# Kernel tuning notes

Hardware: AMD Instinct MI355X
Metric: run time of the kernel (lower is better)

The kernel has to match this reference:

```python
import jax, jax.numpy as jnp
import numpy as np

NEG_SLOPE = 0.2


def gat_conv(x, src, dst, W, a_src, a_dst, b, concat):
    # x: [N, Fin]; W: [H*C, Fin]; a_src/a_dst: [H, C]; b: [H*C] or [C]
    N = x.shape[0]
    H, C = a_src.shape
    h = (x @ W.T).reshape(N, H, C)                      # per-head transform
    s_n = jnp.sum(h * a_src, axis=-1)                   # [N, H]
    d_n = jnp.sum(h * a_dst, axis=-1)                   # [N, H]
    e = jax.nn.leaky_relu(s_n[src] + d_n[dst], NEG_SLOPE)  # [E, H]
    # segment softmax over incoming edges of each destination node
    m = jax.ops.segment_max(e, dst, num_segments=N)
    m = jnp.where(jnp.isfinite(m), m, 0.0)
    ex = jnp.exp(e - m[dst])
    denom = jax.ops.segment_sum(ex, dst, num_segments=N)
    alpha = ex / (denom[dst] + 1e-16)                    # [E, H]
    msg = h[src] * alpha[:, :, None]                     # [E, H, C]
    out = jax.ops.segment_sum(msg, dst, num_segments=N)  # [N, H, C]
    out = out.reshape(N, H * C) if concat else out.mean(axis=1)
    return out + b


def setup_inputs() -> dict:
    key = jax.random.key(0)
    ks = jax.random.split(key, 16)
    N, E, F, C, H = 50000, 800000, 256, 128, 4
    sc = lambda fan_in: 1.0 / np.sqrt(fan_in)
    inp = {
        "x": jax.random.normal(ks[0], (N, F), dtype=jnp.float32),
        "edge_index": jax.random.randint(ks[1], (2, E), 0, N, dtype=jnp.int64),
        # layer 1: F -> H*C (concat)
        "W1": jax.random.normal(ks[2], (H * C, F), jnp.float32) * sc(F),
        "a_src1": jax.random.normal(ks[3], (H, C), jnp.float32) * sc(C),
        "a_dst1": jax.random.normal(ks[4], (H, C), jnp.float32) * sc(C),
        "b1": jnp.zeros((H * C,), jnp.float32),
        # layer 2: H*C -> H*C (concat)
        "W2": jax.random.normal(ks[5], (H * C, H * C), jnp.float32) * sc(H * C),
        "a_src2": jax.random.normal(ks[6], (H, C), jnp.float32) * sc(C),
        "a_dst2": jax.random.normal(ks[7], (H, C), jnp.float32) * sc(C),
        "b2": jnp.zeros((H * C,), jnp.float32),
        # layer 3: H*C -> C (heads=1, concat=False)
        "W3": jax.random.normal(ks[8], (C, H * C), jnp.float32) * sc(H * C),
        "a_src3": jax.random.normal(ks[9], (1, C), jnp.float32) * sc(C),
        "a_dst3": jax.random.normal(ks[10], (1, C), jnp.float32) * sc(C),
        "b3": jnp.zeros((C,), jnp.float32),
        # allocation head: C -> C//2 -> 1
        "Wh1": jax.random.normal(ks[11], (C // 2, C), jnp.float32) * sc(C),
        "bh1": jnp.zeros((C // 2,), jnp.float32),
        "Wh2": jax.random.normal(ks[12], (1, C // 2), jnp.float32) * sc(C // 2),
        "bh2": jnp.zeros((1,), jnp.float32),
    }
    return inp


def reference(x, edge_index, W1, a_src1, a_dst1, b1, W2, a_src2, a_dst2, b2,
              W3, a_src3, a_dst3, b3, Wh1, bh1, Wh2, bh2):
    N = x.shape[0]
    loops = jnp.arange(N, dtype=edge_index.dtype)
    src = jnp.concatenate([edge_index[0], loops])  # self-loops (PyG default)
    dst = jnp.concatenate([edge_index[1], loops])

    h = gat_conv(x, src, dst, W1, a_src1, a_dst1, b1, concat=True)
    h = jax.nn.elu(h)  # dropout is identity at inference
    h = gat_conv(h, src, dst, W2, a_src2, a_dst2, b2, concat=True)
    h = jax.nn.elu(h)
    embeddings = gat_conv(h, src, dst, W3, a_src3, a_dst3, b3, concat=False)

    z = jax.nn.relu(embeddings @ Wh1.T + bh1)
    allocation_scores = jax.nn.sigmoid(z @ Wh2.T + bh2)
    return embeddings, allocation_scores
```

## Files before the change

kernel.cpp:

```cpp
#include <hip/hip_runtime.h>
#include <math.h>

typedef _Float16 f16;
typedef f16 f16x2 __attribute__((ext_vector_type(2)));
typedef f16 f16x4 __attribute__((ext_vector_type(4)));
typedef f16 f16x8 __attribute__((ext_vector_type(8)));
typedef float f32x4 __attribute__((ext_vector_type(4)));

template <int V> struct VecT;
template <> struct VecT<2> { using T = f16 __attribute__((ext_vector_type(2))); };
template <> struct VecT<4> { using T = f16 __attribute__((ext_vector_type(4))); };
template <> struct VecT<8> { using T = f16 __attribute__((ext_vector_type(8))); };

__device__ __forceinline__ unsigned ordf(float f) {
  unsigned u = __float_as_uint(f);
  return (u >> 31) ? ~u : (u | 0x80000000u);
}
__device__ __forceinline__ float unordf(unsigned u) {
  return (u >> 31) ? __uint_as_float(u & 0x7fffffffu) : __uint_as_float(~u);
}


__global__ void k_count(const int* __restrict__ dstArr, int* __restrict__ cnt,
                        int E, int Et) {
  int i = blockIdx.x * blockDim.x + threadIdx.x;
  if (i >= Et) return;
  int d = (i < E) ? dstArr[i] : (i - E);
  atomicAdd(&cnt[d], 1);
}

__global__ __launch_bounds__(256) void k_scanA(const int* __restrict__ cnt,
                                               int* __restrict__ row_ptr,
                                               int* __restrict__ bsum, int n) {
  __shared__ int part[256];
  int t = threadIdx.x;
  int base = blockIdx.x * 1024 + t * 4;
  int4 v = make_int4(0, 0, 0, 0);
  if (base + 3 < n) v = *(const int4*)&cnt[base];
  else {
    if (base + 0 < n) v.x = cnt[base + 0];
    if (base + 1 < n) v.y = cnt[base + 1];
    if (base + 2 < n) v.z = cnt[base + 2];
    if (base + 3 < n) v.w = cnt[base + 3];
  }
  int s = v.x + v.y + v.z + v.w;
  part[t] = s;
  __syncthreads();
  for (int off = 1; off < 256; off <<= 1) {
    int x = (t >= off) ? part[t - off] : 0;
    __syncthreads();
    part[t] += x;
    __syncthreads();
  }
  int p0 = (t == 0) ? 0 : part[t - 1];
  int p1 = p0 + v.x, p2 = p1 + v.y, p3 = p2 + v.z;
  if (base + 0 < n) row_ptr[base + 0] = p0;
  if (base + 1 < n) row_ptr[base + 1] = p1;
  if (base + 2 < n) row_ptr[base + 2] = p2;
  if (base + 3 < n) row_ptr[base + 3] = p3;
  if (t == 255) bsum[blockIdx.x] = part[255];
}

__global__ __launch_bounds__(1024) void k_scanB(int* __restrict__ bsum, int nb) {
  __shared__ int part[1024];
  int t = threadIdx.x;
  int v = (t < nb) ? bsum[t] : 0;
  part[t] = v;
  __syncthreads();
  for (int off = 1; off < 1024; off <<= 1) {
    int x = (t >= off) ? part[t - off] : 0;
    __syncthreads();
    part[t] += x;
    __syncthreads();
  }
  if (t < nb) bsum[t] = (t == 0) ? 0 : part[t - 1];
  if (t == 1023) bsum[nb] = part[1023];
}

__global__ void k_scanC(int* __restrict__ row_ptr, int* __restrict__ cursor,
                        const int* __restrict__ bsum, int n, int nb) {
  int i = blockIdx.x * blockDim.x + threadIdx.x;
  if (i < n) {
    int v = row_ptr[i] + bsum[i >> 10];
    row_ptr[i] = v;
    cursor[i] = v;
  }
  if (i == n) row_ptr[n] = bsum[nb];
}

__global__ void k_fill(const int* __restrict__ dstArr,
                       const int* __restrict__ srcArr, int* __restrict__ cursor,
                       int* __restrict__ esrc, int E, int Et) {
  int i = blockIdx.x * blockDim.x + threadIdx.x;
  if (i >= Et) return;
  int d, s;
  if (i < E) { d = dstArr[i]; s = srcArr[i]; }
  else       { d = i - E; s = d; }
  int pos = atomicAdd(&cursor[d], 1);
  esrc[pos] = s;
}

__global__ void k_f2h4(const float* s0, f16* d0, int n0,
                       const float* s1, f16* d1, int n1,
                       const float* s2, f16* d2, int n2,
                       const float* s3, f16* d3, int n3) {
  int i = blockIdx.x * blockDim.x + threadIdx.x;
  const float* s; f16* d;
  if (i < n0) { s = s0; d = d0; }
  else if ((i -= n0) < n1) { s = s1; d = d1; }
  else if ((i -= n1) < n2) { s = s2; d = d2; }
  else if ((i -= n2) < n3) { s = s3; d = d3; }
  else return;
  float4 v = ((const float4*)s)[i];
  union { f16 h[4]; double dd; } u;
  u.h[0] = (f16)v.x; u.h[1] = (f16)v.y; u.h[2] = (f16)v.z; u.h[3] = (f16)v.w;
  ((double*)d)[i] = u.dd;
}

__global__ __launch_bounds__(256) void k_hgemm_nt(
    const f16* __restrict__ A, const f16* __restrict__ B,
    f16* __restrict__ C, int M, int Nn, int K, int nbx,
    const float* __restrict__ a_src, const float* __restrict__ a_dst,
    float* __restrict__ sArr, float* __restrict__ dArr,
    unsigned* __restrict__ gmaxU, int H) {
  __shared__ f16 As[3 * 4096];
  __shared__ f16 Bs[3 * 4096];
  int tid = threadIdx.x;
  int wave = tid >> 6, lane = tid & 63;
  int quad = lane >> 4, l16 = lane & 15;

  int nwg = gridDim.x;
  int orig = blockIdx.x;
  int q = nwg >> 3, r = nwg & 7;
  int xcd = orig & 7, pos = orig >> 3;
  int swz = (xcd < r) ? (xcd * (q + 1) + pos)
                      : (r * (q + 1) + (xcd - r) * q + pos);
  int bx = swz % nbx;
  int by = swz / nbx;
  int m0 = by * 128, n0 = bx * 128;
  int wm = (wave & 1) * 64, wn = (wave >> 1) * 64;

  int lr = lane >> 2;
  int lc = lane & 3;
  int chunk = lc ^ ((lr >> 1) & 3);
  int rb0 = wave * 16;
  int rb1 = 64 + wave * 16;
  int ga0 = m0 + rb0 + lr; if (ga0 >= M) ga0 = M - 1;
  int ga1 = m0 + rb1 + lr; if (ga1 >= M) ga1 = M - 1;
  const f16* gA0 = A + (size_t)ga0 * K + chunk * 8;
  const f16* gA1 = A + (size_t)ga1 * K + chunk * 8;
  const f16* gB0 = B + (size_t)(n0 + rb0 + lr) * K + chunk * 8;
  const f16* gB1 = B + (size_t)(n0 + rb1 + lr) * K + chunk * 8;

  int rsw = (quad ^ ((l16 >> 1) & 3)) * 8;
  const f16* Ard[4];
  const f16* Brd[4];
#pragma unroll
  for (int i = 0; i < 4; ++i) {
    Ard[i] = &As[(wm + i * 16 + l16) * 32 + rsw];
    Brd[i] = &Bs[(wn + i * 16 + l16) * 32 + rsw];
  }

  f32x4 acc[4][4];
#pragma unroll
  for (int i = 0; i < 4; ++i)
#pragma unroll
    for (int j = 0; j < 4; ++j) acc[i][j] = (f32x4)(0.f);

#define GLDS(gp, lp)                                                     \
  __builtin_amdgcn_global_load_lds(                                      \
      (const __attribute__((address_space(1))) void*)(gp),               \
      (__attribute__((address_space(3))) void*)(lp), 16, 0, 0)
#define STAGE(buf, kk)                                                   \
  do {                                                                   \
    GLDS(gA0 + (kk), As + (buf) * 4096 + rb0 * 32);                      \
    GLDS(gA1 + (kk), As + (buf) * 4096 + rb1 * 32);                      \
    GLDS(gB0 + (kk), Bs + (buf) * 4096 + rb0 * 32);                      \
    GLDS(gB1 + (kk), Bs + (buf) * 4096 + rb1 * 32);                      \
  } while (0)
#define COMPUTE(bufidx)                                                       \
  do {                                                                        \
    f16x8 af[4], bf[4];                                                       \
    _Pragma("unroll") for (int i_ = 0; i_ < 4; ++i_)                          \
        af[i_] = *(const f16x8*)(Ard[i_] + (bufidx) * 4096);                  \
    _Pragma("unroll") for (int j_ = 0; j_ < 4; ++j_)                          \
        bf[j_] = *(const f16x8*)(Brd[j_] + (bufidx) * 4096);                  \
    _Pragma("unroll") for (int i_ = 0; i_ < 4; ++i_)                          \
        _Pragma("unroll") for (int j_ = 0; j_ < 4; ++j_)                      \
            acc[i_][j_] = __builtin_amdgcn_mfma_f32_16x16x32_f16(             \
                af[i_], bf[j_], acc[i_][j_], 0, 0, 0);                        \
  } while (0)

  int nt = K >> 5;
  STAGE(0, 0);
  STAGE(1, 32);
  int cur = 0, sb = 2;
  for (int t = 0; t + 2 < nt; ++t) {
    STAGE(sb, (t + 2) << 5);
    asm volatile("s_waitcnt vmcnt(8)\n\ts_barrier" ::: "memory");
    COMPUTE(cur);
    asm volatile("s_barrier" ::: "memory");
    cur = (cur == 2) ? 0 : cur + 1;
    sb = (sb == 2) ? 0 : sb + 1;
  }
  asm volatile("s_waitcnt vmcnt(4)\n\ts_barrier" ::: "memory");
  COMPUTE(cur);
  asm volatile("s_barrier" ::: "memory");
  cur = (cur == 2) ? 0 : cur + 1;
  asm volatile("s_waitcnt vmcnt(0)\n\ts_barrier" ::: "memory");
  COMPUTE(cur);
#undef STAGE
#undef GLDS
#undef COMPUTE

#pragma unroll
  for (int i = 0; i < 4; ++i) {
#pragma unroll
    for (int r = 0; r < 4; ++r) {
      int m = m0 + wm + i * 16 + quad * 4 + r;
      if (m < M) {
        f16* Cp = C + (size_t)m * Nn + n0 + wn + l16;
#pragma unroll
        for (int j = 0; j < 4; ++j) Cp[j * 16] = (f16)acc[i][j][r];
      }
    }
  }

  float av[4], ad[4];
#pragma unroll
  for (int j = 0; j < 4; ++j) {
    int col = n0 + wn + l16 + j * 16;
    av[j] = a_src[col];
    ad[j] = a_dst[col];
  }
  float sp[16], dp[16];
#pragma unroll
  for (int i = 0; i < 4; ++i)
#pragma unroll
    for (int r = 0; r < 4; ++r) {
      float ss = 0.f, dd = 0.f;
#pragma unroll
      for (int j = 0; j < 4; ++j) {
        ss += acc[i][j][r] * av[j];
        dd += acc[i][j][r] * ad[j];
      }
#pragma unroll
      for (int msk = 1; msk < 16; msk <<= 1) {
        ss += __shfl_xor(ss, msk);
        dd += __shfl_xor(dd, msk);
      }
      sp[i * 4 + r] = ss;
      dp[i * 4 + r] = dd;
    }

  __syncthreads();
  float* fb = (float*)As;
  int wv = wn >> 6;
  if (l16 == 0) {
#pragma unroll
    for (int i = 0; i < 4; ++i)
#pragma unroll
      for (int r = 0; r < 4; ++r) {
        int row = wm + i * 16 + quad * 4 + r;
        fb[wv * 128 + row] = sp[i * 4 + r];
        fb[256 + wv * 128 + row] = dp[i * 4 + r];
      }
  }
  __syncthreads();
  float sval = -3.0e38f;
  if (tid < 128) {
    int m = m0 + tid;
    if (m < M) {
      float s = fb[tid] + fb[128 + tid];
      float d = fb[256 + tid] + fb[384 + tid];
      int head = n0 >> 7;
      sArr[(size_t)m * H + head] = s;
      dArr[(size_t)m * H + head] = d;
      sval = s;
    }
  }
  float mx = sval;
#pragma unroll
  for (int msk = 32; msk; msk >>= 1) mx = fmaxf(mx, __shfl_xor(mx, msk));
  __syncthreads();
  if (lane == 0) fb[512 + wave] = mx;
  __syncthreads();
  if (tid == 0) {
    float m01 = fmaxf(fb[512], fb[513]);
    atomicMax(&gmaxU[n0 >> 7], ordf(m01));
  }
}

template <int HH, int CT, bool DOELU, typename OutT>
__global__ __launch_bounds__(256) void k_aggregate(
    const f16* __restrict__ hin, const float* __restrict__ sArr,
    const float* __restrict__ dArr, const int* __restrict__ row_ptr,
    const int* __restrict__ esrc, const unsigned* __restrict__ gmaxU,
    const float* __restrict__ bias, OutT* __restrict__ outp, int N, int E) {
  constexpr int VEC = (HH == 1) ? 4 : (CT / 64);
  constexpr int CPER = CT / HH;
  using gvec = typename VecT<VEC>::T;

  __shared__ int2 pairs[4][HH * 66];

  int wave = threadIdx.x >> 6;
  int lane = threadIdx.x & 63;
  int n = blockIdx.x * 4 + wave;
  if (n >= N) return;
  int e0 = row_ptr[n];
  int deg = row_ptr[n + 1] - e0;

  const int myhead = (HH == 1) ? 0 : (lane * VEC) / CPER;
  const int l32 = lane & 31, half = lane >> 5;
  const int laneByte = (HH == 1) ? l32 * 8 : lane * VEC * 2;

  float dloc[HH], mn[HH];
#pragma unroll
  for (int h = 0; h < HH; ++h) {
    dloc[h] = dArr[n * HH + h];
    float m = unordf(gmaxU[h]) + dloc[h];
    mn[h] = (m > 0.f) ? m : 0.2f * m;
  }

  float acc[VEC];
#pragma unroll
  for (int k = 0; k < VEC; ++k) acc[k] = 0.f;
  float dsum[HH];
#pragma unroll
  for (int h = 0; h < HH; ++h) dsum[h] = 0.f;

  int2* pw = &pairs[wave][0];
  const int2* pr = &pairs[wave][myhead * 66];

#define PIDX(g, j) ((HH == 1) ? ((g) * 8 + (j) * 2 + half) : ((g) * 4 + (j)))
#define LOADG(VB, WB, g)                                                      \
  do {                                                                        \
    _Pragma("unroll") for (int j_ = 0; j_ < 4; ++j_) {                        \
      int2 p_ = pr[PIDX(g, j_)];                                              \
      WB[j_] = __int_as_float(p_.y);                                          \
      VB[j_] = *(const gvec*)((const char*)hin + (unsigned)(p_.x + laneByte));\
    }                                                                         \
  } while (0)

#define FMAG(VB, WB)                                                          \
  do {                                                                        \
    _Pragma("unroll") for (int j_ = 0; j_ < 4; ++j_)                          \
        _Pragma("unroll") for (int k_ = 0; k_ < VEC; ++k_)                    \
            acc[k_] += WB[j_] * (float)VB[j_][k_];                            \
  } while (0)

  for (int base = 0; base < deg; base += 64) {
    int cn = min(64, deg - base);

    int soff = 0;
    float w_l[HH];
#pragma unroll
    for (int h = 0; h < HH; ++h) w_l[h] = 0.f;
    if (lane < cn) {
      int s = esrc[e0 + base + lane];
      soff = s * (CT * 2);
      if (HH == 4) {
        float4 sv = ((const float4*)sArr)[s];
        float svv[4] = {sv.x, sv.y, sv.z, sv.w};
#pragma unroll
        for (int h = 0; h < 4; ++h) {
          float e = svv[h] + dloc[h];
          e = (e > 0.f) ? e : 0.2f * e;
          w_l[h] = __expf(e - mn[h]);
        }
      } else {
        float e = sArr[s] + dloc[0];
        e = (e > 0.f) ? e : 0.2f * e;
        w_l[0] = __expf(e - mn[0]);
      }
    }
#pragma unroll
    for (int h = 0; h < HH; ++h) dsum[h] += w_l[h];

#pragma unroll
    for (int h = 0; h < HH; ++h)
      pw[h * 66 + lane] = make_int2(soff, __float_as_int(w_l[h]));
    asm volatile("s_waitcnt lgkmcnt(0)" ::: "memory");

    int cng = (HH == 1) ? ((cn + 7) >> 3) : ((cn + 3) >> 2);
    gvec vA[4], vB[4];
    float wA[4], wB[4];
    LOADG(vA, wA, 0);
    int g = 0;
    while (g + 2 < cng) {
      LOADG(vB, wB, g + 1);
      FMAG(vA, wA);
      LOADG(vA, wA, g + 2);
      FMAG(vB, wB);
      g += 2;
    }
    if (g + 1 < cng) {
      LOADG(vB, wB, g + 1);
      FMAG(vA, wA);
      FMAG(vB, wB);
    } else {
      FMAG(vA, wA);
    }
  }
#undef LOADG
#undef FMAG
#undef PIDX

  if (HH == 1) {
#pragma unroll
    for (int k = 0; k < VEC; ++k) acc[k] += __shfl_xor(acc[k], 32);
  }

  float dn;
  if (HH == 4) {
    float t0 = dsum[0], t1 = dsum[1], t2 = dsum[2], t3 = dsum[3];
#pragma unroll
    for (int m = 1; m < 64; m <<= 1) {
      t0 += __shfl_xor(t0, m);
      t1 += __shfl_xor(t1, m);
      t2 += __shfl_xor(t2, m);
      t3 += __shfl_xor(t3, m);
    }
    dn = (myhead < 2) ? (myhead == 0 ? t0 : t1) : (myhead == 2 ? t2 : t3);
  } else {
    float t0 = dsum[0];
#pragma unroll
    for (int m = 1; m < 64; m <<= 1) t0 += __shfl_xor(t0, m);
    dn = t0;
  }
  dn += 1e-16f;

  if (HH == 1) {
    if (lane < 32) {
      struct alignas(16) OutV { OutT v[4]; } ov;
#pragma unroll
      for (int k = 0; k < 4; ++k) {
        float v = acc[k] / dn + bias[l32 * 4 + k];
        if (DOELU) v = (v > 0.f) ? v : expm1f(v);
        ov.v[k] = (OutT)v;
      }
      *(OutV*)(outp + (size_t)n * CT + l32 * 4) = ov;
    }
  } else {
    struct alignas(sizeof(OutT) * VEC) OutV { OutT v[VEC]; } ov;
#pragma unroll
    for (int k = 0; k < VEC; ++k) {
      float v = acc[k] / dn + bias[lane * VEC + k];
      if (DOELU) v = (v > 0.f) ? v : expm1f(v);
      ov.v[k] = (OutT)v;
    }
    *(OutV*)(outp + (size_t)n * CT + lane * VEC) = ov;
  }
}

__global__ __launch_bounds__(256) void k_head(
    const float* __restrict__ emb, const float* __restrict__ Wh1,
    const float* __restrict__ bh1, const float* __restrict__ Wh2,
    const float* __restrict__ bh2, float* __restrict__ scores, int N) {
  __shared__ float w1s[64 * 132];
  __shared__ float w2s[64];
  __shared__ float b1s[64];
  int t = threadIdx.x;
  for (int i = t; i < 64 * 32; i += 256) {
    int r = i >> 5, c4 = i & 31;
    float4 v = ((const float4*)Wh1)[i];
    *(float4*)&w1s[r * 132 + c4 * 4] = v;
  }
  if (t < 64) { w2s[t] = Wh2[t]; b1s[t] = bh1[t]; }
  __syncthreads();
  float b2v = bh2[0];
  int wave = t >> 6, lane = t & 63;
  int gw = blockIdx.x * 4 + wave;
  int nw = gridDim.x * 4;
  for (int n = gw; n < N; n += nw) {
    float2 xv = ((const float2*)(emb + (size_t)n * 128))[lane];
    float z = b1s[lane];
#pragma unroll
    for (int j = 0; j < 32; ++j) {
      float4 w = *(const float4*)&w1s[lane * 132 + 4 * j];
      float a0 = __shfl(xv.x, 2 * j);
      float a1 = __shfl(xv.y, 2 * j);
      float a2 = __shfl(xv.x, 2 * j + 1);
      float a3 = __shfl(xv.y, 2 * j + 1);
      z += w.x * a0 + w.y * a1 + w.z * a2 + w.w * a3;
    }
    z = fmaxf(z, 0.f);
    float v = z * w2s[lane];
#pragma unroll
    for (int off = 32; off; off >>= 1) v += __shfl_down(v, off);
    if (lane == 0) scores[n] = 1.f / (1.f + __expf(-(v + b2v)));
  }
}


extern "C" void kernel_launch(void* const* d_in, const int* in_sizes, int n_in,
                              void* d_out, int out_size, void* d_ws, size_t ws_size,
                              hipStream_t stream) {
  const float* x   = (const float*)d_in[0];
  const int*   ei  = (const int*)d_in[1];
  const float* W1  = (const float*)d_in[2];
  const float* as1 = (const float*)d_in[3];
  const float* ad1 = (const float*)d_in[4];
  const float* b1  = (const float*)d_in[5];
  const float* W2  = (const float*)d_in[6];
  const float* as2 = (const float*)d_in[7];
  const float* ad2 = (const float*)d_in[8];
  const float* b2  = (const float*)d_in[9];
  const float* W3  = (const float*)d_in[10];
  const float* as3 = (const float*)d_in[11];
  const float* ad3 = (const float*)d_in[12];
  const float* b3  = (const float*)d_in[13];
  const float* Wh1 = (const float*)d_in[14];
  const float* bh1 = (const float*)d_in[15];
  const float* Wh2 = (const float*)d_in[16];
  const float* bh2 = (const float*)d_in[17];
  float* out = (float*)d_out;

  const int F = 256, HC = 512, H = 4, C = 128;
  const int N = in_sizes[0] / F;
  const int E = in_sizes[1] / 2;
  const int Et = E + N;
  const int* srcArr = ei;
  const int* dstArr = ei + E;

  char* ws = (char*)d_ws;
  size_t off = 0;
  auto alloc = [&](size_t bytes) -> void* {
    void* p = ws + off;
    off += (bytes + 255) & ~(size_t)255;
    return p;
  };
  f16*   h16    = (f16*)alloc((size_t)N * HC * 2);
  f16*   hAgg   = (f16*)alloc((size_t)N * HC * 2);
  f16*   xh     = (f16*)alloc((size_t)N * F * 2);
  f16*   W1h    = (f16*)alloc((size_t)HC * F * 2);
  f16*   W2h    = (f16*)alloc((size_t)HC * HC * 2);
  f16*   W3h    = (f16*)alloc((size_t)C * HC * 2);
  int* row_ptr  = (int*)alloc((size_t)(N + 1) * 4);
  char* zr      = (char*)alloc((size_t)N * 4 + 64);
  int* cnt      = (int*)zr;
  unsigned* gm1 = (unsigned*)(zr + (size_t)N * 4);
  unsigned* gm2 = gm1 + 4;
  unsigned* gm3 = gm1 + 8;
  int* cursor   = (int*)alloc((size_t)N * 4);
  int* esrc     = (int*)alloc((size_t)Et * 4);
  float* sArr   = (float*)alloc((size_t)N * H * 4);
  float* dArr   = (float*)alloc((size_t)N * H * 4);
  int* bsum     = (int*)alloc((size_t)1028 * 4);
  (void)ws_size; (void)n_in; (void)out_size;

  hipMemsetAsync(zr, 0, (size_t)N * 4 + 64, stream);
  int eb = (Et + 255) / 256;
  int nb = (N + 1023) / 1024;
  k_count<<<eb, 256, 0, stream>>>(dstArr, cnt, E, Et);
  k_scanA<<<nb, 256, 0, stream>>>(cnt, row_ptr, bsum, N);
  k_scanB<<<1, 1024, 0, stream>>>(bsum, nb);
  k_scanC<<<(N + 256) / 256, 256, 0, stream>>>(row_ptr, cursor, bsum, N, nb);
  k_fill<<<eb, 256, 0, stream>>>(dstArr, srcArr, cursor, esrc, E, Et);

  int c0 = N * F / 4, c1 = HC * F / 4, c2 = HC * HC / 4, c3 = C * HC / 4;
  int ctot = c0 + c1 + c2 + c3;
  k_f2h4<<<(ctot + 255) / 256, 256, 0, stream>>>(x, xh, c0, W1, W1h, c1,
                                                 W2, W2h, c2, W3, W3h, c3);

  int aggGrid = (N + 3) / 4;
  int mblk = (N + 127) / 128;
  int nblk1 = 4 * mblk;
  int nblk3 = mblk;

  k_hgemm_nt<<<nblk1, 256, 0, stream>>>(xh, W1h, h16, N, HC, F, 4,
                                        as1, ad1, sArr, dArr, gm1, H);
  k_aggregate<4, 512, true, f16><<<aggGrid, 256, 0, stream>>>(
      h16, sArr, dArr, row_ptr, esrc, gm1, b1, hAgg, N, E);

  k_hgemm_nt<<<nblk1, 256, 0, stream>>>(hAgg, W2h, h16, N, HC, HC, 4,
                                        as2, ad2, sArr, dArr, gm2, H);
  k_aggregate<4, 512, true, f16><<<aggGrid, 256, 0, stream>>>(
      h16, sArr, dArr, row_ptr, esrc, gm2, b2, hAgg, N, E);

  k_hgemm_nt<<<nblk3, 256, 0, stream>>>(hAgg, W3h, h16, N, C, HC, 1,
                                        as3, ad3, sArr, dArr, gm3, 1);
  k_aggregate<1, 128, false, float><<<aggGrid, 256, 0, stream>>>(
      h16, sArr, dArr, row_ptr, esrc, gm3, b3, out, N, E);

  k_head<<<512, 256, 0, stream>>>(out, Wh1, bh1, Wh2, bh2, out + (size_t)N * C, N);
}
```

Measured before the change: 743.5 us.

## Reorder layer-1 GAT to aggregate raw features before the linear transform

For layer 1, the attention logits are computed directly from x by folding a_src/a_dst into W1 (k_ws, k_sd). The raw 256-wide features are then aggregated per head into a [N,4,256] buffer (k_aggx). The per-head GEMM then runs on the aggregated features, with bias and ELU fused into its epilogue. Gathering 256-wide fp16 rows instead of 512-wide transformed rows cuts gather traffic, but it writes and reads a 1024-wide intermediate and adds several kernels.

```diff
diff --git a/kernel.cpp b/kernel.cpp
--- a/kernel.cpp
+++ b/kernel.cpp
@@ -117,10 +117,197 @@
   ((double*)d)[i] = u.dd;
 }
 
+__global__ __launch_bounds__(256) void k_ws(const float* __restrict__ W1,
+                                            const float* __restrict__ as,
+                                            const float* __restrict__ ad,
+                                            float* __restrict__ wsb) {
+  int b = blockIdx.x;
+  int which = b >> 2, h = b & 3;
+  int f = threadIdx.x;
+  const float* av = (which ? ad : as) + h * 128;
+  float acc = 0.f;
+  for (int c = 0; c < 128; ++c)
+    acc += av[c] * W1[(size_t)(h * 128 + c) * 256 + f];
+  wsb[(which * 4 + h) * 256 + f] = acc;
+}
+
+__global__ __launch_bounds__(256) void k_sd(
+    const f16* __restrict__ xh, const float* __restrict__ wsb,
+    float* __restrict__ sArr, float* __restrict__ dArr,
+    unsigned* __restrict__ gmaxU, int N) {
+  __shared__ float mred[4][8];
+  int tid = threadIdx.x;
+  int wave = tid >> 6, lane = tid & 63;
+  float wreg[8][4];
+#pragma unroll
+  for (int q = 0; q < 8; ++q) {
+    float4 w = *(const float4*)&wsb[q * 256 + lane * 4];
+    wreg[q][0] = w.x; wreg[q][1] = w.y; wreg[q][2] = w.z; wreg[q][3] = w.w;
+  }
+  int qsel = lane & 7;
+  float rmax = -3.0e38f;
+  int step = gridDim.x * 4;
+  for (int n = blockIdx.x * 4 + wave; n < N; n += step) {
+    f16x4 xr = *(const f16x4*)(xh + (size_t)n * 256 + lane * 4);
+    float xv[4];
+#pragma unroll
+    for (int k = 0; k < 4; ++k) xv[k] = (float)xr[k];
+    float p[8];
+#pragma unroll
+    for (int q = 0; q < 8; ++q)
+      p[q] = xv[0] * wreg[q][0] + xv[1] * wreg[q][1] +
+             xv[2] * wreg[q][2] + xv[3] * wreg[q][3];
+#pragma unroll
+    for (int m = 1; m < 8; m <<= 1)
+#pragma unroll
+      for (int q = 0; q < 8; ++q) p[q] += __shfl_xor(p[q], m);
+    float s01 = (qsel & 1) ? p[1] : p[0], s23 = (qsel & 1) ? p[3] : p[2];
+    float s45 = (qsel & 1) ? p[5] : p[4], s67 = (qsel & 1) ? p[7] : p[6];
+    float t0 = (qsel & 2) ? s23 : s01, t1 = (qsel & 2) ? s67 : s45;
+    float v = (qsel & 4) ? t1 : t0;
+    v += __shfl_xor(v, 8);
+    v += __shfl_xor(v, 16);
+    v += __shfl_xor(v, 32);
+    if (lane < 4) {
+      sArr[(size_t)n * 4 + lane] = v;
+      rmax = fmaxf(rmax, v);
+    } else if (lane < 8) {
+      dArr[(size_t)n * 4 + (lane - 4)] = v;
+    }
+  }
+  if (lane < 4) mred[wave][lane] = rmax;
+  __syncthreads();
+  if (tid < 4) {
+    float m = fmaxf(fmaxf(mred[0][tid], mred[1][tid]),
+                    fmaxf(mred[2][tid], mred[3][tid]));
+    atomicMax(&gmaxU[tid], ordf(m));
+  }
+}
+
+__global__ __launch_bounds__(256) void k_aggx(
+    const f16* __restrict__ xh, const float* __restrict__ sArr,
+    const float* __restrict__ dArr, const int* __restrict__ row_ptr,
+    const int* __restrict__ esrc, const unsigned* __restrict__ gmaxU,
+    f16* __restrict__ outp, int N, int E) {
+  __shared__ int soffA[4][72];
+  __shared__ float4 w4A[4][64];
+  int wave = threadIdx.x >> 6;
+  int lane = threadIdx.x & 63;
+  int n = blockIdx.x * 4 + wave;
+  if (n >= N) return;
+  int e0 = row_ptr[n];
+  int deg = row_ptr[n + 1] - e0;
+
+  float4 dl4 = ((const float4*)dArr)[n];
+  float dloc[4] = {dl4.x, dl4.y, dl4.z, dl4.w};
+  float mn[4];
+#pragma unroll
+  for (int h = 0; h < 4; ++h) {
+    float m = unordf(gmaxU[h]) + dloc[h];
+    mn[h] = (m > 0.f) ? m : 0.2f * m;
+  }
+
+  float acc[4][4];
+#pragma unroll
+  for (int h = 0; h < 4; ++h)
+#pragma unroll
+    for (int k = 0; k < 4; ++k) acc[h][k] = 0.f;
+  float dsum[4] = {0.f, 0.f, 0.f, 0.f};
+
+  int* so = soffA[wave];
+  float4* wp = w4A[wave];
+
+#define LOADX(VB, WB, g)                                                    \
+  do {                                                                      \
+    _Pragma("unroll") for (int j_ = 0; j_ < 4; ++j_) {                      \
+      int sidx_ = (g) * 4 + j_;                                             \
+      WB[j_] = wp[sidx_];                                                   \
+      VB[j_] = *(const f16x4*)((const char*)xh +                            \
+                               (unsigned)(so[sidx_] + lane * 8));           \
+    }                                                                       \
+  } while (0)
+
+#define FMAX4(VB, WB)                                                       \
+  do {                                                                      \
+    _Pragma("unroll") for (int j_ = 0; j_ < 4; ++j_)                        \
+        _Pragma("unroll") for (int k_ = 0; k_ < 4; ++k_) {                  \
+          float xv_ = (float)VB[j_][k_];                                    \
+          acc[0][k_] += WB[j_].x * xv_;                                     \
+          acc[1][k_] += WB[j_].y * xv_;                                     \
+          acc[2][k_] += WB[j_].z * xv_;                                     \
+          acc[3][k_] += WB[j_].w * xv_;                                     \
+        }                                                                   \
+  } while (0)
+
+  for (int base = 0; base < deg; base += 64) {
+    int cn = min(64, deg - base);
+    int soff = 0;
+    float w_l[4] = {0.f, 0.f, 0.f, 0.f};
+    if (lane < cn) {
+      int s = esrc[e0 + base + lane];
+      soff = s * 512;
+      float4 sv = ((const float4*)sArr)[s];
+      float svv[4] = {sv.x, sv.y, sv.z, sv.w};
+#pragma unroll
+      for (int h = 0; h < 4; ++h) {
+        float e = svv[h] + dloc[h];
+        e = (e > 0.f) ? e : 0.2f * e;
+        w_l[h] = __expf(e - mn[h]);
+      }
+    }
+#pragma unroll
+    for (int h = 0; h < 4; ++h) dsum[h] += w_l[h];
+    so[lane] = soff;
+    wp[lane] = make_float4(w_l[0], w_l[1], w_l[2], w_l[3]);
+    asm volatile("s_waitcnt lgkmcnt(0)" ::: "memory");
+
+    int cng = (cn + 3) >> 2;
+    f16x4 vA[4], vB[4];
+    float4 wA[4], wB[4];
+    LOADX(vA, wA, 0);
+    int g = 0;
+    while (g + 2 < cng) {
+      LOADX(vB, wB, g + 1);
+      FMAX4(vA, wA);
+      LOADX(vA, wA, g + 2);
+      FMAX4(vB, wB);
+      g += 2;
+    }
+    if (g + 1 < cng) {
+      LOADX(vB, wB, g + 1);
+      FMAX4(vA, wA);
+      FMAX4(vB, wB);
+    } else {
+      FMAX4(vA, wA);
+    }
+  }
+#undef LOADX
+#undef FMAX4
+
+  float t0 = dsum[0], t1 = dsum[1], t2 = dsum[2], t3 = dsum[3];
+#pragma unroll
+  for (int m = 1; m < 64; m <<= 1) {
+    t0 += __shfl_xor(t0, m);
+    t1 += __shfl_xor(t1, m);
+    t2 += __shfl_xor(t2, m);
+    t3 += __shfl_xor(t3, m);
+  }
+  float dnv[4] = {t0 + 1e-16f, t1 + 1e-16f, t2 + 1e-16f, t3 + 1e-16f};
+#pragma unroll
+  for (int h = 0; h < 4; ++h) {
+    f16x4 ov;
+#pragma unroll
+    for (int k = 0; k < 4; ++k) ov[k] = (f16)(acc[h][k] / dnv[h]);
+    *(f16x4*)(outp + (size_t)n * 1024 + h * 256 + lane * 4) = ov;
+  }
+}
+
+template <int EPI>
 __global__ __launch_bounds__(256) void k_hgemm_nt(
     const f16* __restrict__ A, const f16* __restrict__ B,
-    f16* __restrict__ C, int M, int Nn, int K, int nbx,
+    f16* __restrict__ C, int M, int Nn, int K, int lda, int hstride, int nbx,
     const float* __restrict__ a_src, const float* __restrict__ a_dst,
+    const float* __restrict__ bias,
     float* __restrict__ sArr, float* __restrict__ dArr,
     unsigned* __restrict__ gmaxU, int H) {
   __shared__ f16 As[3 * 4096];
@@ -139,6 +326,7 @@
   int by = swz / nbx;
   int m0 = by * 128, n0 = bx * 128;
   int wm = (wave & 1) * 64, wn = (wave >> 1) * 64;
+  int headOff = (n0 >> 7) * hstride;
 
   int lr = lane >> 2;
   int lc = lane & 3;
@@ -147,8 +335,8 @@
   int rb1 = 64 + wave * 16;
   int ga0 = m0 + rb0 + lr; if (ga0 >= M) ga0 = M - 1;
   int ga1 = m0 + rb1 + lr; if (ga1 >= M) ga1 = M - 1;
-  const f16* gA0 = A + (size_t)ga0 * K + chunk * 8;
-  const f16* gA1 = A + (size_t)ga1 * K + chunk * 8;
+  const f16* gA0 = A + (size_t)ga0 * lda + headOff + chunk * 8;
+  const f16* gA1 = A + (size_t)ga1 * lda + headOff + chunk * 8;
   const f16* gB0 = B + (size_t)(n0 + rb0 + lr) * K + chunk * 8;
   const f16* gB1 = B + (size_t)(n0 + rb1 + lr) * K + chunk * 8;
 
@@ -213,6 +401,29 @@
 #undef GLDS
 #undef COMPUTE
 
+  if (EPI == 1) {
+    float bcol[4];
+#pragma unroll
+    for (int j = 0; j < 4; ++j) bcol[j] = bias[n0 + wn + l16 + j * 16];
+#pragma unroll
+    for (int i = 0; i < 4; ++i) {
+#pragma unroll
+      for (int r = 0; r < 4; ++r) {
+        int m = m0 + wm + i * 16 + quad * 4 + r;
+        if (m < M) {
+          f16* Cp = C + (size_t)m * Nn + n0 + wn + l16;
+#pragma unroll
+          for (int j = 0; j < 4; ++j) {
+            float v = acc[i][j][r] + bcol[j];
+            v = (v > 0.f) ? v : expm1f(v);
+            Cp[j * 16] = (f16)v;
+          }
+        }
+      }
+    }
+    return;
+  }
+
 #pragma unroll
   for (int i = 0; i < 4; ++i) {
 #pragma unroll
@@ -530,12 +741,14 @@
     off += (bytes + 255) & ~(size_t)255;
     return p;
   };
-  f16*   h16    = (f16*)alloc((size_t)N * HC * 2);
+  f16*   xagg4  = (f16*)alloc((size_t)N * 1024 * 2);
+  f16*   h16    = xagg4;
   f16*   hAgg   = (f16*)alloc((size_t)N * HC * 2);
   f16*   xh     = (f16*)alloc((size_t)N * F * 2);
   f16*   W1h    = (f16*)alloc((size_t)HC * F * 2);
   f16*   W2h    = (f16*)alloc((size_t)HC * HC * 2);
   f16*   W3h    = (f16*)alloc((size_t)C * HC * 2);
+  float* wsb    = (float*)alloc((size_t)8 * 256 * 4);
   int* row_ptr  = (int*)alloc((size_t)(N + 1) * 4);
   char* zr      = (char*)alloc((size_t)N * 4 + 64);
   int* cnt      = (int*)zr;
@@ -568,18 +781,23 @@
   int nblk1 = 4 * mblk;
   int nblk3 = mblk;
 
-  k_hgemm_nt<<<nblk1, 256, 0, stream>>>(xh, W1h, h16, N, HC, F, 4,
-                                        as1, ad1, sArr, dArr, gm1, H);
-  k_aggregate<4, 512, true, f16><<<aggGrid, 256, 0, stream>>>(
-      h16, sArr, dArr, row_ptr, esrc, gm1, b1, hAgg, N, E);
-
-  k_hgemm_nt<<<nblk1, 256, 0, stream>>>(hAgg, W2h, h16, N, HC, HC, 4,
-                                        as2, ad2, sArr, dArr, gm2, H);
+  k_ws<<<8, 256, 0, stream>>>(W1, as1, ad1, wsb);
+  k_sd<<<1024, 256, 0, stream>>>(xh, wsb, sArr, dArr, gm1, N);
+  k_aggx<<<aggGrid, 256, 0, stream>>>(xh, sArr, dArr, row_ptr, esrc, gm1,
+                                      xagg4, N, E);
+  k_hgemm_nt<1><<<nblk1, 256, 0, stream>>>(
+      xagg4, W1h, hAgg, N, HC, F, 1024, 256, 4,
+      nullptr, nullptr, b1, nullptr, nullptr, nullptr, H);
+
+  k_hgemm_nt<0><<<nblk1, 256, 0, stream>>>(
+      hAgg, W2h, h16, N, HC, HC, HC, 0, 4,
+      as2, ad2, nullptr, sArr, dArr, gm2, H);
   k_aggregate<4, 512, true, f16><<<aggGrid, 256, 0, stream>>>(
       h16, sArr, dArr, row_ptr, esrc, gm2, b2, hAgg, N, E);
 
-  k_hgemm_nt<<<nblk3, 256, 0, stream>>>(hAgg, W3h, h16, N, C, HC, 1,
-                                        as3, ad3, sArr, dArr, gm3, 1);
+  k_hgemm_nt<0><<<nblk3, 256, 0, stream>>>(
+      hAgg, W3h, h16, N, C, HC, HC, 0, 1,
+      as3, ad3, nullptr, sArr, dArr, gm3, 1);
   k_aggregate<1, 128, false, float><<<aggGrid, 256, 0, stream>>>(
       h16, sArr, dArr, row_ptr, esrc, gm3, b3, out, N, E);
 
```

Result: faster. 726.3 us (-2.3%).
